# Kernel tuning notes

Hardware: AMD Instinct MI355X
Metric: run time of the kernel (lower is better)

The kernel has to match this reference:

```python
import jax, jax.numpy as jnp
import numpy as np

T, N, L = 2000, 128, 250
H, K, V, A = 512, 128, 128, 64  # hidden_dim, key_size, value_size, alphabet_size


def _lstm_cell(x, h, c, W_ih, W_hh, b_ih, b_hh):
    # PyTorch LSTMCell gate order: i, f, g, o
    gates = x @ W_ih.T + b_ih + h @ W_hh.T + b_hh
    i, f, g, o = jnp.split(gates, 4, axis=-1)
    c_new = jax.nn.sigmoid(f) * c + jax.nn.sigmoid(i) * jnp.tanh(g)
    h_new = jax.nn.sigmoid(o) * jnp.tanh(c_new)
    return h_new, c_new


def setup_inputs() -> dict:
    ks = jax.random.split(jax.random.key(0), 16)
    u = lambda k, shape, s: jax.random.uniform(k, shape, jnp.float32, -s, s)
    sH = 1.0 / np.sqrt(H)
    sK = 1.0 / np.sqrt(K)
    return {
        "key": jax.random.normal(ks[0], (T, N, K), jnp.float32),
        "values": jax.random.normal(ks[1], (T, N, V), jnp.float32),
        "lens": jax.random.randint(ks[2], (N,), 1, T + 1),
        "text": jax.random.randint(ks[3], (N, L), 0, A),
        "emb": jax.random.normal(ks[4], (A, H), jnp.float32).at[0].set(0.0),
        "W_ih1": u(ks[5], (4 * H, H + V), sH),
        "W_hh1": u(ks[6], (4 * H, H), sH),
        "b_ih1": u(ks[7], (4 * H,), sH),
        "b_hh1": u(ks[8], (4 * H,), sH),
        "W_ih2": u(ks[9], (4 * K, H), sK),
        "W_hh2": u(ks[10], (4 * K, K), sK),
        "b_ih2": u(ks[11], (4 * K,), sK),
        "b_hh2": u(ks[12], (4 * K,), sK),
        "W_mos": u(ks[13], (A, K + V), 1.0 / np.sqrt(K + V)),
        "b_mos": u(ks[14], (A,), 1.0 / np.sqrt(K + V)),
    }


def reference(key, values, lens, text, emb, W_ih1, W_hh1, b_ih1, b_hh1,
              W_ih2, W_hh2, b_ih2, b_hh2, W_mos, b_mos):
    batch = key.shape[1]
    # padding_idx=0: zero embedding for token 0
    embeddings = emb[text] * (text != 0)[..., None].astype(emb.dtype)  # (N,L,H)
    emb_seq = jnp.transpose(embeddings, (1, 0, 2))                     # (L,N,H)
    mask = jnp.arange(key.shape[0])[None, :] >= lens[:, None]          # (N,T)

    def step(carry, e):
        h1, c1, h2, c2, ctx = carry
        inp = jnp.concatenate([e, ctx], axis=1)                # (N,H+V)
        h1, c1 = _lstm_cell(inp, h1, c1, W_ih1, W_hh1, b_ih1, b_hh1)
        h2, c2 = _lstm_cell(h1, h2, c2, W_ih2, W_hh2, b_ih2, b_hh2)
        scores = jnp.einsum('tnk,nk->nt', key, h2)             # (N,T)
        scores = jnp.where(mask, -1e9, scores)
        attn = jax.nn.softmax(scores, axis=1)
        ctx = jnp.einsum('nt,tnv->nv', attn, values)           # (N,V)
        pred = jnp.concatenate([h2, ctx], axis=1) @ W_mos.T + b_mos  # (N,A)
        return (h1, c1, h2, c2, ctx), pred

    z1 = jnp.zeros((batch, H), key.dtype)
    z2 = jnp.zeros((batch, K), key.dtype)
    init = (z1, z1, z2, z2, values[0])
    _, preds = jax.lax.scan(step, init, emb_seq)               # (L,N,A)
    return jnp.transpose(preds, (1, 0, 2))                     # (N,L,A)
```

## Files before the change

### kernel.cpp

```cpp
#include <hip/hip_runtime.h>
#include <hip/hip_bf16.h>
#include <math.h>

#define T_ENC 2000
#define NB    128
#define LDEC  250
#define HDIM  512
#define KDIM  128
#define VDIM  128
#define ADIM  64
#define TC    100
#define NC    20
#define K1    1152
#define K2    640
#define N1    2048
#define N2    512

typedef __attribute__((ext_vector_type(8))) short bf16x8;
typedef __attribute__((ext_vector_type(4))) float f32x4;
typedef unsigned short u16;

__device__ __forceinline__ u16 f2bf(float x) {
    unsigned int b = __float_as_uint(x);
    b += 0x7fffu + ((b >> 16) & 1u);
    return (u16)(b >> 16);
}
__device__ __forceinline__ float bfhi2f(unsigned int u) {
    return __uint_as_float(u << 16);
}
__device__ __forceinline__ f32x4 mfma16(bf16x8 a, bf16x8 b, f32x4 c) {
    return __builtin_amdgcn_mfma_f32_16x16x32_bf16(a, b, c, 0, 0, 0);
}


__global__ void cvt_tr(const float* __restrict__ src, u16* __restrict__ dst) {
    size_t total = (size_t)T_ENC * NB * 128;
    for (size_t idx = (size_t)blockIdx.x * 256 + threadIdx.x; idx < total;
         idx += (size_t)gridDim.x * 256) {
        int t = idx >> 14;
        int n = (idx >> 7) & 127;
        int d = idx & 127;
        dst[((size_t)n * T_ENC + t) * 128 + d] = f2bf(src[idx]);
    }
}

__global__ void prep_emb(const int* __restrict__ text, const float* __restrict__ emb,
                         u16* __restrict__ Ehi, u16* __restrict__ Elo) {
    size_t total = (size_t)LDEC * NB * HDIM;
    for (size_t idx = (size_t)blockIdx.x * 256 + threadIdx.x; idx < total;
         idx += (size_t)gridDim.x * 256) {
        int t = idx >> 16;
        int n = (idx >> 9) & 127;
        int d = idx & 511;
        int tok = text[n * LDEC + t];
        float v = tok ? emb[(size_t)tok * HDIM + d] : 0.f;
        u16 hi = f2bf(v);
        Ehi[idx] = hi;
        Elo[idx] = f2bf(v - bfhi2f((unsigned int)hi));
    }
}

__global__ void prep_w1(const float* __restrict__ Wih, const float* __restrict__ Whh,
                        const float* __restrict__ bi, const float* __restrict__ bh,
                        u16* __restrict__ Whi, u16* __restrict__ Wlo,
                        float* __restrict__ bsum) {
    size_t total = (size_t)N1 * K1;
    for (size_t idx = (size_t)blockIdx.x * 256 + threadIdx.x; idx < total;
         idx += (size_t)gridDim.x * 256) {
        int c = idx / K1, k = idx % K1;
        float w = (k < 640) ? Wih[(size_t)c * 640 + k] : Whh[(size_t)c * 512 + (k - 640)];
        u16 hi = f2bf(w);
        Whi[idx] = hi;
        Wlo[idx] = f2bf(w - bfhi2f((unsigned int)hi));
    }
    int i = blockIdx.x * 256 + threadIdx.x;
    if (i < N1) bsum[i] = bi[i] + bh[i];
}

__global__ void prep_w2(const float* __restrict__ Wih, const float* __restrict__ Whh,
                        const float* __restrict__ bi, const float* __restrict__ bh,
                        u16* __restrict__ Whi, u16* __restrict__ Wlo,
                        float* __restrict__ bsum) {
    size_t total = (size_t)N2 * K2;
    for (size_t idx = (size_t)blockIdx.x * 256 + threadIdx.x; idx < total;
         idx += (size_t)gridDim.x * 256) {
        int c = idx / K2, k = idx % K2;
        float w = (k < 512) ? Wih[(size_t)c * 512 + k] : Whh[(size_t)c * 128 + (k - 512)];
        u16 hi = f2bf(w);
        Whi[idx] = hi;
        Wlo[idx] = f2bf(w - bfhi2f((unsigned int)hi));
    }
    int i = blockIdx.x * 256 + threadIdx.x;
    if (i < N2) bsum[i] = bi[i] + bh[i];
}

__global__ void init_state(float* c1, u16* h1hi, u16* h1lo,
                           float* c2, u16* h2hi, u16* h2lo,
                           u16* cxhi, u16* cxlo, const float* __restrict__ values) {
    int i = blockIdx.x * 256 + threadIdx.x;
    c1[i] = 0.f; h1hi[i] = 0; h1lo[i] = 0;
    if (i < NB * KDIM) {
        c2[i] = 0.f; h2hi[i] = 0; h2lo[i] = 0;
        float v = values[i];
        u16 hi = f2bf(v);
        cxhi[i] = hi; cxlo[i] = f2bf(v - bfhi2f((unsigned int)hi));
    }
}


__global__ __launch_bounds__(256) void lstm1_mfma(
    const u16* __restrict__ Ehi, const u16* __restrict__ Elo,
    const u16* __restrict__ cxhi, const u16* __restrict__ cxlo,
    const u16* __restrict__ h1hi, const u16* __restrict__ h1lo,
    const u16* __restrict__ W1hi, const u16* __restrict__ W1lo,
    float* __restrict__ gpart, int t)
{
    int tid = threadIdx.x, lane = tid & 63, wid = tid >> 6;
    int wn = wid >> 1, wj = wid & 1;
    int l15 = lane & 15, l4 = lane >> 4;
    int n0 = blockIdx.x * 64 + wn * 32;
    int j0 = blockIdx.y * 32 + wj * 16;
    int ks = blockIdx.z;
    int kbeg = ks * 288, kend = kbeg + 288;

    f32x4 zero = {0.f, 0.f, 0.f, 0.f};
    f32x4 acc[2][4];
#pragma unroll
    for (int m = 0; m < 2; ++m)
#pragma unroll
        for (int g = 0; g < 4; ++g) acc[m][g] = zero;

    size_t brow[4];
#pragma unroll
    for (int g = 0; g < 4; ++g) brow[g] = (size_t)(g * 512 + j0 + l15) * K1;
    int row0 = n0 + l15, row1 = n0 + 16 + l15;
    const u16* Et_hi = Ehi + (size_t)t * (NB * HDIM);
    const u16* Et_lo = Elo + (size_t)t * (NB * HDIM);

    for (int kk = kbeg; kk < kend; kk += 32) {
        int kb = kk + l4 * 8;
        const u16 *pah, *pal; size_t ao0, ao1;
        if (kk < 512) {
            pah = Et_hi; pal = Et_lo;
            ao0 = (size_t)row0 * 512 + kb; ao1 = (size_t)row1 * 512 + kb;
        } else if (kk < 640) {
            pah = cxhi; pal = cxlo;
            ao0 = (size_t)row0 * 128 + (kb - 512); ao1 = (size_t)row1 * 128 + (kb - 512);
        } else {
            pah = h1hi; pal = h1lo;
            ao0 = (size_t)row0 * 512 + (kb - 640); ao1 = (size_t)row1 * 512 + (kb - 640);
        }
        bf16x8 a0h = *(const bf16x8*)(pah + ao0);
        bf16x8 a0l = *(const bf16x8*)(pal + ao0);
        bf16x8 a1h = *(const bf16x8*)(pah + ao1);
        bf16x8 a1l = *(const bf16x8*)(pal + ao1);
#pragma unroll
        for (int g = 0; g < 4; ++g) {
            bf16x8 bh = *(const bf16x8*)(W1hi + brow[g] + kb);
            bf16x8 bl = *(const bf16x8*)(W1lo + brow[g] + kb);
            acc[0][g] = mfma16(a0h, bh, acc[0][g]);
            acc[0][g] = mfma16(a0h, bl, acc[0][g]);
            acc[0][g] = mfma16(a0l, bh, acc[0][g]);
            acc[1][g] = mfma16(a1h, bh, acc[1][g]);
            acc[1][g] = mfma16(a1h, bl, acc[1][g]);
            acc[1][g] = mfma16(a1l, bh, acc[1][g]);
        }
    }
#pragma unroll
    for (int mi = 0; mi < 2; ++mi)
#pragma unroll
        for (int g = 0; g < 4; ++g)
#pragma unroll
            for (int r = 0; r < 4; ++r) {
                int row = n0 + mi * 16 + l4 * 4 + r;
                gpart[((size_t)ks * NB + row) * N1 + g * 512 + j0 + l15] = acc[mi][g][r];
            }
}

__global__ __launch_bounds__(256) void pw1(
    const float* __restrict__ gpart, const float* __restrict__ bsum,
    float* __restrict__ c1, u16* __restrict__ h1hi, u16* __restrict__ h1lo)
{
    int idx = blockIdx.x * 256 + threadIdx.x;
    int n = idx >> 9, j = idx & 511;
    float g[4];
#pragma unroll
    for (int gi = 0; gi < 4; ++gi) {
        int c = gi * 512 + j;
        float s = bsum[c];
#pragma unroll
        for (int ks = 0; ks < 4; ++ks) s += gpart[((size_t)ks * NB + n) * N1 + c];
        g[gi] = s;
    }
    float cc = c1[idx];
    float i_ = 1.f / (1.f + expf(-g[0]));
    float f_ = 1.f / (1.f + expf(-g[1]));
    float g_ = tanhf(g[2]);
    float o_ = 1.f / (1.f + expf(-g[3]));
    float cn = f_ * cc + i_ * g_;
    c1[idx] = cn;
    float h = o_ * tanhf(cn);
    u16 hi = f2bf(h);
    h1hi[idx] = hi;
    h1lo[idx] = f2bf(h - bfhi2f((unsigned int)hi));
}

__global__ __launch_bounds__(256) void lstm2_mfma(
    const u16* __restrict__ h1hi, const u16* __restrict__ h1lo,
    const u16* __restrict__ h2hi, const u16* __restrict__ h2lo,
    const u16* __restrict__ W2hi, const u16* __restrict__ W2lo,
    float* __restrict__ gpart)
{
    int tid = threadIdx.x, lane = tid & 63, wid = tid >> 6;
    int wn = wid >> 1, wj = wid & 1;
    int l15 = lane & 15, l4 = lane >> 4;
    int n0 = blockIdx.x * 64 + wn * 32;
    int j0 = blockIdx.y * 32 + wj * 16;
    int ks = blockIdx.z;
    int kbeg = ks * 160, kend = kbeg + 160;

    f32x4 zero = {0.f, 0.f, 0.f, 0.f};
    f32x4 acc[2][4];
#pragma unroll
    for (int m = 0; m < 2; ++m)
#pragma unroll
        for (int g = 0; g < 4; ++g) acc[m][g] = zero;

    size_t brow[4];
#pragma unroll
    for (int g = 0; g < 4; ++g) brow[g] = (size_t)(g * 128 + j0 + l15) * K2;
    int row0 = n0 + l15, row1 = n0 + 16 + l15;

    for (int kk = kbeg; kk < kend; kk += 32) {
        int kb = kk + l4 * 8;
        const u16 *pah, *pal; size_t ao0, ao1;
        if (kk < 512) {
            pah = h1hi; pal = h1lo;
            ao0 = (size_t)row0 * 512 + kb; ao1 = (size_t)row1 * 512 + kb;
        } else {
            pah = h2hi; pal = h2lo;
            ao0 = (size_t)row0 * 128 + (kb - 512); ao1 = (size_t)row1 * 128 + (kb - 512);
        }
        bf16x8 a0h = *(const bf16x8*)(pah + ao0);
        bf16x8 a0l = *(const bf16x8*)(pal + ao0);
        bf16x8 a1h = *(const bf16x8*)(pah + ao1);
        bf16x8 a1l = *(const bf16x8*)(pal + ao1);
#pragma unroll
        for (int g = 0; g < 4; ++g) {
            bf16x8 bh = *(const bf16x8*)(W2hi + brow[g] + kb);
            bf16x8 bl = *(const bf16x8*)(W2lo + brow[g] + kb);
            acc[0][g] = mfma16(a0h, bh, acc[0][g]);
            acc[0][g] = mfma16(a0h, bl, acc[0][g]);
            acc[0][g] = mfma16(a0l, bh, acc[0][g]);
            acc[1][g] = mfma16(a1h, bh, acc[1][g]);
            acc[1][g] = mfma16(a1h, bl, acc[1][g]);
            acc[1][g] = mfma16(a1l, bh, acc[1][g]);
        }
    }
#pragma unroll
    for (int mi = 0; mi < 2; ++mi)
#pragma unroll
        for (int g = 0; g < 4; ++g)
#pragma unroll
            for (int r = 0; r < 4; ++r) {
                int row = n0 + mi * 16 + l4 * 4 + r;
                gpart[((size_t)ks * NB + row) * N2 + g * 128 + j0 + l15] = acc[mi][g][r];
            }
}

__global__ __launch_bounds__(256) void pw2(
    const float* __restrict__ gpart, const float* __restrict__ bsum,
    float* __restrict__ c2, float* __restrict__ h2f,
    u16* __restrict__ h2hi, u16* __restrict__ h2lo)
{
    int idx = blockIdx.x * 256 + threadIdx.x;
    int n = idx >> 7, j = idx & 127;
    float g[4];
#pragma unroll
    for (int gi = 0; gi < 4; ++gi) {
        int c = gi * 128 + j;
        float s = bsum[c];
#pragma unroll
        for (int ks = 0; ks < 4; ++ks) s += gpart[((size_t)ks * NB + n) * N2 + c];
        g[gi] = s;
    }
    float cc = c2[idx];
    float i_ = 1.f / (1.f + expf(-g[0]));
    float f_ = 1.f / (1.f + expf(-g[1]));
    float g_ = tanhf(g[2]);
    float o_ = 1.f / (1.f + expf(-g[3]));
    float cn = f_ * cc + i_ * g_;
    c2[idx] = cn;
    float h = o_ * tanhf(cn);
    h2f[idx] = h;
    u16 hi = f2bf(h);
    h2hi[idx] = hi;
    h2lo[idx] = f2bf(h - bfhi2f((unsigned int)hi));
}

__global__ __launch_bounds__(256) void attn_partial(
    const u16* __restrict__ kbf, const u16* __restrict__ vbf,
    const float* __restrict__ h2f, const int* __restrict__ lens,
    float* __restrict__ pmax, float* __restrict__ psum, float* __restrict__ pctx)
{
    int n = blockIdx.x, c = blockIdx.y, t0 = c * TC;
    int tid = threadIdx.x, lane = tid & 63, w = tid >> 6;
    int l15 = lane & 15, l4 = lane >> 4;
    __shared__ float pls[TC];
    __shared__ float red[8];
    __shared__ float cpart[4][VDIM];
    int len = lens[n];

    float h2r[8];
    {
        const float* hp = h2f + n * 128 + l15 * 8;
#pragma unroll
        for (int j = 0; j < 8; ++j) h2r[j] = hp[j];
    }

    const u16* kb_ = kbf + (size_t)n * T_ENC * 128;
    for (int q = w; q < 25; q += 4) {
        int tl = 4 * q + l4;
        int t = t0 + tl;
        uint4 u = *(const uint4*)(kb_ + (size_t)t * 128 + l15 * 8);
        float s = 0.f;
        s = fmaf(bfhi2f(u.x & 0xffffu), h2r[0], s);
        s = fmaf(bfhi2f(u.x >> 16),     h2r[1], s);
        s = fmaf(bfhi2f(u.y & 0xffffu), h2r[2], s);
        s = fmaf(bfhi2f(u.y >> 16),     h2r[3], s);
        s = fmaf(bfhi2f(u.z & 0xffffu), h2r[4], s);
        s = fmaf(bfhi2f(u.z >> 16),     h2r[5], s);
        s = fmaf(bfhi2f(u.w & 0xffffu), h2r[6], s);
        s = fmaf(bfhi2f(u.w >> 16),     h2r[7], s);
        s += __shfl_xor(s, 1, 64);
        s += __shfl_xor(s, 2, 64);
        s += __shfl_xor(s, 4, 64);
        s += __shfl_xor(s, 8, 64);
        if (t >= len) s = -1e30f;
        if (l15 == 0) pls[tl] = s;
    }
    __syncthreads();

    float m = -1e30f;
    for (int i = tid; i < TC; i += 256) m = fmaxf(m, pls[i]);
    for (int k = 32; k >= 1; k >>= 1) m = fmaxf(m, __shfl_xor(m, k, 64));
    if (lane == 0) red[w] = m;
    __syncthreads();
    m = fmaxf(fmaxf(red[0], red[1]), fmaxf(red[2], red[3]));
    bool empty = (m <= -1e29f);

    float ssum = 0.f;
    for (int i = tid; i < TC; i += 256) {
        float pv = empty ? 0.f : expf(pls[i] - m);
        pls[i] = pv;
        ssum += pv;
    }
    __syncthreads();
    for (int k = 32; k >= 1; k >>= 1) ssum += __shfl_xor(ssum, k, 64);
    if (lane == 0) red[4 + w] = ssum;
    __syncthreads();
    if (tid == 0) {
        pmax[n * NC + c] = empty ? -1e30f : m;
        psum[n * NC + c] = red[4] + red[5] + red[6] + red[7];
    }

    const u16* vb_ = vbf + (size_t)n * T_ENC * 128;
    int l5 = lane >> 5, l31 = lane & 31;
    float a4[4] = {0.f, 0.f, 0.f, 0.f};
    for (int p = w; p < 50; p += 4) {
        int tl = 2 * p + l5;
        int t = t0 + tl;
        float pv = pls[tl];
        uint2 u = *(const uint2*)(vb_ + (size_t)t * 128 + l31 * 4);
        a4[0] = fmaf(pv, bfhi2f(u.x & 0xffffu), a4[0]);
        a4[1] = fmaf(pv, bfhi2f(u.x >> 16),     a4[1]);
        a4[2] = fmaf(pv, bfhi2f(u.y & 0xffffu), a4[2]);
        a4[3] = fmaf(pv, bfhi2f(u.y >> 16),     a4[3]);
    }
#pragma unroll
    for (int j = 0; j < 4; ++j) a4[j] += __shfl_xor(a4[j], 32, 64);
    if (lane < 32) {
#pragma unroll
        for (int j = 0; j < 4; ++j) cpart[w][l31 * 4 + j] = a4[j];
    }
    __syncthreads();
    if (tid < 128)
        pctx[((size_t)n * NC + c) * VDIM + tid] =
            cpart[0][tid] + cpart[1][tid] + cpart[2][tid] + cpart[3][tid];
}

__global__ __launch_bounds__(64) void combine_pred(
    const float* __restrict__ pmax, const float* __restrict__ psum,
    const float* __restrict__ pctx, const float* __restrict__ h2f,
    u16* __restrict__ cxhi, u16* __restrict__ cxlo,
    const float* __restrict__ W_mos, const float* __restrict__ b_mos,
    float* __restrict__ out, int t)
{
    int n = blockIdx.x;
    int lane = threadIdx.x;

    float m = (lane < NC) ? pmax[n * NC + lane] : -1e30f;
    for (int k = 32; k >= 1; k >>= 1) m = fmaxf(m, __shfl_xor(m, k, 64));
    float s = (lane < NC) ? psum[n * NC + lane] * expf(pmax[n * NC + lane] - m) : 0.f;
    for (int k = 32; k >= 1; k >>= 1) s += __shfl_xor(s, k, 64);
    float inv = 1.f / s;

    __shared__ float xcat[2 * KDIM];
#pragma unroll
    for (int v2 = 0; v2 < 2; ++v2) {
        int v = lane + v2 * 64;
        float acc = 0.f;
        for (int c = 0; c < NC; ++c) {
            float e = expf(pmax[n * NC + c] - m);
            acc += pctx[((size_t)n * NC + c) * VDIM + v] * e;
        }
        acc *= inv;
        u16 hi = f2bf(acc);
        cxhi[n * 128 + v] = hi;
        cxlo[n * 128 + v] = f2bf(acc - bfhi2f((unsigned int)hi));
        xcat[KDIM + v] = acc;
    }
    xcat[lane] = h2f[n * 128 + lane];
    xcat[64 + lane] = h2f[n * 128 + 64 + lane];
    __syncthreads();

    float acc = b_mos[lane];
    const float* wr = W_mos + lane * (2 * KDIM);
#pragma unroll 4
    for (int i = 0; i < 2 * KDIM; ++i) acc += xcat[i] * wr[i];
    out[((size_t)n * LDEC + t) * ADIM + lane] = acc;
}


extern "C" void kernel_launch(void* const* d_in, const int* in_sizes, int n_in,
                              void* d_out, int out_size, void* d_ws, size_t ws_size,
                              hipStream_t stream)
{
    const float* key    = (const float*)d_in[0];
    const float* values = (const float*)d_in[1];
    const int*   lens   = (const int*)d_in[2];
    const int*   text   = (const int*)d_in[3];
    const float* emb    = (const float*)d_in[4];
    const float* W_ih1  = (const float*)d_in[5];
    const float* W_hh1  = (const float*)d_in[6];
    const float* b_ih1  = (const float*)d_in[7];
    const float* b_hh1  = (const float*)d_in[8];
    const float* W_ih2  = (const float*)d_in[9];
    const float* W_hh2  = (const float*)d_in[10];
    const float* b_ih2  = (const float*)d_in[11];
    const float* b_hh2  = (const float*)d_in[12];
    const float* W_mos  = (const float*)d_in[13];
    const float* b_mos  = (const float*)d_in[14];
    float* out = (float*)d_out;

    char* base = (char*)d_ws;
    size_t off = 0;
    auto alloc = [&](size_t bytes) -> char* {
        char* r = base + off;
        off += (bytes + 255) & ~(size_t)255;
        return r;
    };
    u16* kbf  = (u16*)alloc((size_t)T_ENC * NB * 128 * 2);
    u16* vbf  = (u16*)alloc((size_t)T_ENC * NB * 128 * 2);
    u16* Ehi  = (u16*)alloc((size_t)LDEC * NB * HDIM * 2);
    u16* Elo  = (u16*)alloc((size_t)LDEC * NB * HDIM * 2);
    u16* W1hi = (u16*)alloc((size_t)N1 * K1 * 2);
    u16* W1lo = (u16*)alloc((size_t)N1 * K1 * 2);
    u16* W2hi = (u16*)alloc((size_t)N2 * K2 * 2);
    u16* W2lo = (u16*)alloc((size_t)N2 * K2 * 2);
    float* bsum1 = (float*)alloc(N1 * 4);
    float* bsum2 = (float*)alloc(N2 * 4);
    float* gpart1 = (float*)alloc((size_t)4 * NB * N1 * 4);
    float* gpart2 = (float*)alloc((size_t)4 * NB * N2 * 4);
    u16* h1hiA = (u16*)alloc(NB * HDIM * 2);
    u16* h1loA = (u16*)alloc(NB * HDIM * 2);
    u16* h1hiB = (u16*)alloc(NB * HDIM * 2);
    u16* h1loB = (u16*)alloc(NB * HDIM * 2);
    u16* h2hiA = (u16*)alloc(NB * KDIM * 2);
    u16* h2loA = (u16*)alloc(NB * KDIM * 2);
    u16* h2hiB = (u16*)alloc(NB * KDIM * 2);
    u16* h2loB = (u16*)alloc(NB * KDIM * 2);
    float* c1  = (float*)alloc(NB * HDIM * 4);
    float* c2  = (float*)alloc(NB * KDIM * 4);
    float* h2f = (float*)alloc(NB * KDIM * 4);
    u16* cxhi = (u16*)alloc(NB * VDIM * 2);
    u16* cxlo = (u16*)alloc(NB * VDIM * 2);
    float* pmax = (float*)alloc(NB * NC * 4);
    float* psum = (float*)alloc(NB * NC * 4);
    float* pctx = (float*)alloc((size_t)NB * NC * VDIM * 4);
    (void)ws_size; (void)in_sizes; (void)n_in; (void)out_size;

    cvt_tr<<<4096, 256, 0, stream>>>(key, kbf);
    cvt_tr<<<4096, 256, 0, stream>>>(values, vbf);
    prep_emb<<<4096, 256, 0, stream>>>(text, emb, Ehi, Elo);
    prep_w1<<<2048, 256, 0, stream>>>(W_ih1, W_hh1, b_ih1, b_hh1, W1hi, W1lo, bsum1);
    prep_w2<<<512, 256, 0, stream>>>(W_ih2, W_hh2, b_ih2, b_hh2, W2hi, W2lo, bsum2);
    init_state<<<256, 256, 0, stream>>>(c1, h1hiA, h1loA, c2, h2hiA, h2loA,
                                        cxhi, cxlo, values);

    for (int t = 0; t < LDEC; ++t) {
        u16* h1hi_i = (t & 1) ? h1hiB : h1hiA;
        u16* h1lo_i = (t & 1) ? h1loB : h1loA;
        u16* h1hi_o = (t & 1) ? h1hiA : h1hiB;
        u16* h1lo_o = (t & 1) ? h1loA : h1loB;
        u16* h2hi_i = (t & 1) ? h2hiB : h2hiA;
        u16* h2lo_i = (t & 1) ? h2loB : h2loA;
        u16* h2hi_o = (t & 1) ? h2hiA : h2hiB;
        u16* h2lo_o = (t & 1) ? h2loA : h2loB;

        lstm1_mfma<<<dim3(2, 16, 4), 256, 0, stream>>>(
            Ehi, Elo, cxhi, cxlo, h1hi_i, h1lo_i, W1hi, W1lo, gpart1, t);
        pw1<<<256, 256, 0, stream>>>(gpart1, bsum1, c1, h1hi_o, h1lo_o);
        lstm2_mfma<<<dim3(2, 4, 4), 256, 0, stream>>>(
            h1hi_o, h1lo_o, h2hi_i, h2lo_i, W2hi, W2lo, gpart2);
        pw2<<<64, 256, 0, stream>>>(gpart2, bsum2, c2, h2f, h2hi_o, h2lo_o);
        attn_partial<<<dim3(NB, NC), 256, 0, stream>>>(kbf, vbf, h2f, lens,
                                                       pmax, psum, pctx);
        combine_pred<<<NB, 64, 0, stream>>>(pmax, psum, pctx, h2f,
                                            cxhi, cxlo, W_mos, b_mos, out, t);
    }
}
```

Before: 18.60 ms.

## Fuse LSTM gate GEMMs with pointwise cell update via in-block split-K reduction

Each LSTM layer's split-K GEMM now splits K across the four waves inside one block and reduces the partial sums in shared memory. The same block then applies the gate nonlinearities and updates the cell state. This removes the pw1 and pw2 launches and the global gpart round-trip on every decoder step, at the cost of a different grid shape and one block barrier. The attention partial kernel also exits early for chunks that lie entirely past the sequence length, which skips key loads and dot products for padded time steps.

```diff
diff --git a/kernel.cpp b/kernel.cpp
--- a/kernel.cpp
+++ b/kernel.cpp
@@ -108,20 +108,21 @@
 }
 
 
-__global__ __launch_bounds__(256) void lstm1_mfma(
+__global__ __launch_bounds__(256) void lstm1_fused(
     const u16* __restrict__ Ehi, const u16* __restrict__ Elo,
     const u16* __restrict__ cxhi, const u16* __restrict__ cxlo,
-    const u16* __restrict__ h1hi, const u16* __restrict__ h1lo,
+    const u16* __restrict__ h1hi_in, const u16* __restrict__ h1lo_in,
     const u16* __restrict__ W1hi, const u16* __restrict__ W1lo,
-    float* __restrict__ gpart, int t)
+    const float* __restrict__ bsum,
+    float* __restrict__ c1, u16* __restrict__ h1hi_o, u16* __restrict__ h1lo_o,
+    int t)
 {
-    int tid = threadIdx.x, lane = tid & 63, wid = tid >> 6;
-    int wn = wid >> 1, wj = wid & 1;
+    __shared__ float red[4][32][64];
+    int tid = threadIdx.x, lane = tid & 63, wk = tid >> 6;
     int l15 = lane & 15, l4 = lane >> 4;
-    int n0 = blockIdx.x * 64 + wn * 32;
-    int j0 = blockIdx.y * 32 + wj * 16;
-    int ks = blockIdx.z;
-    int kbeg = ks * 288, kend = kbeg + 288;
+    int n0 = blockIdx.x * 32;
+    int j0 = blockIdx.y * 16;
+    int kbeg = wk * 288, kend = kbeg + 288;
 
     f32x4 zero = {0.f, 0.f, 0.f, 0.f};
     f32x4 acc[2][4];
@@ -147,7 +148,7 @@
             pah = cxhi; pal = cxlo;
             ao0 = (size_t)row0 * 128 + (kb - 512); ao1 = (size_t)row1 * 128 + (kb - 512);
         } else {
-            pah = h1hi; pal = h1lo;
+            pah = h1hi_in; pal = h1lo_in;
             ao0 = (size_t)row0 * 512 + (kb - 640); ao1 = (size_t)row1 * 512 + (kb - 640);
         }
         bf16x8 a0h = *(const bf16x8*)(pah + ao0);
@@ -171,53 +172,49 @@
 #pragma unroll
         for (int g = 0; g < 4; ++g)
 #pragma unroll
-            for (int r = 0; r < 4; ++r) {
-                int row = n0 + mi * 16 + l4 * 4 + r;
-                gpart[((size_t)ks * NB + row) * N1 + g * 512 + j0 + l15] = acc[mi][g][r];
-            }
-}
-
-__global__ __launch_bounds__(256) void pw1(
-    const float* __restrict__ gpart, const float* __restrict__ bsum,
-    float* __restrict__ c1, u16* __restrict__ h1hi, u16* __restrict__ h1lo)
+            for (int r = 0; r < 4; ++r)
+                red[wk][mi * 16 + l4 * 4 + r][g * 16 + l15] = acc[mi][g][r];
+    __syncthreads();
+
+    for (int cell = tid; cell < 512; cell += 256) {
+        int nl = cell >> 4, jl = cell & 15;
+        float g[4];
+#pragma unroll
+        for (int gi = 0; gi < 4; ++gi) {
+            float s = bsum[gi * 512 + j0 + jl];
+#pragma unroll
+            for (int w = 0; w < 4; ++w) s += red[w][nl][gi * 16 + jl];
+            g[gi] = s;
+        }
+        int idx = (n0 + nl) * HDIM + j0 + jl;
+        float cc = c1[idx];
+        float i_ = 1.f / (1.f + expf(-g[0]));
+        float f_ = 1.f / (1.f + expf(-g[1]));
+        float g_ = tanhf(g[2]);
+        float o_ = 1.f / (1.f + expf(-g[3]));
+        float cn = f_ * cc + i_ * g_;
+        c1[idx] = cn;
+        float h = o_ * tanhf(cn);
+        u16 hi = f2bf(h);
+        h1hi_o[idx] = hi;
+        h1lo_o[idx] = f2bf(h - bfhi2f((unsigned int)hi));
+    }
+}
+
+__global__ __launch_bounds__(256) void lstm2_fused(
+    const u16* __restrict__ h1hi, const u16* __restrict__ h1lo,
+    const u16* __restrict__ h2hi_in, const u16* __restrict__ h2lo_in,
+    const u16* __restrict__ W2hi, const u16* __restrict__ W2lo,
+    const float* __restrict__ bsum,
+    float* __restrict__ c2, float* __restrict__ h2f,
+    u16* __restrict__ h2hi_o, u16* __restrict__ h2lo_o)
 {
-    int idx = blockIdx.x * 256 + threadIdx.x;
-    int n = idx >> 9, j = idx & 511;
-    float g[4];
-#pragma unroll
-    for (int gi = 0; gi < 4; ++gi) {
-        int c = gi * 512 + j;
-        float s = bsum[c];
-#pragma unroll
-        for (int ks = 0; ks < 4; ++ks) s += gpart[((size_t)ks * NB + n) * N1 + c];
-        g[gi] = s;
-    }
-    float cc = c1[idx];
-    float i_ = 1.f / (1.f + expf(-g[0]));
-    float f_ = 1.f / (1.f + expf(-g[1]));
-    float g_ = tanhf(g[2]);
-    float o_ = 1.f / (1.f + expf(-g[3]));
-    float cn = f_ * cc + i_ * g_;
-    c1[idx] = cn;
-    float h = o_ * tanhf(cn);
-    u16 hi = f2bf(h);
-    h1hi[idx] = hi;
-    h1lo[idx] = f2bf(h - bfhi2f((unsigned int)hi));
-}
-
-__global__ __launch_bounds__(256) void lstm2_mfma(
-    const u16* __restrict__ h1hi, const u16* __restrict__ h1lo,
-    const u16* __restrict__ h2hi, const u16* __restrict__ h2lo,
-    const u16* __restrict__ W2hi, const u16* __restrict__ W2lo,
-    float* __restrict__ gpart)
-{
-    int tid = threadIdx.x, lane = tid & 63, wid = tid >> 6;
-    int wn = wid >> 1, wj = wid & 1;
+    __shared__ float red[4][32][64];
+    int tid = threadIdx.x, lane = tid & 63, wk = tid >> 6;
     int l15 = lane & 15, l4 = lane >> 4;
-    int n0 = blockIdx.x * 64 + wn * 32;
-    int j0 = blockIdx.y * 32 + wj * 16;
-    int ks = blockIdx.z;
-    int kbeg = ks * 160, kend = kbeg + 160;
+    int n0 = blockIdx.x * 32;
+    int j0 = blockIdx.y * 16;
+    int kbeg = wk * 160, kend = kbeg + 160;
 
     f32x4 zero = {0.f, 0.f, 0.f, 0.f};
     f32x4 acc[2][4];
@@ -238,7 +235,7 @@
             pah = h1hi; pal = h1lo;
             ao0 = (size_t)row0 * 512 + kb; ao1 = (size_t)row1 * 512 + kb;
         } else {
-            pah = h2hi; pal = h2lo;
+            pah = h2hi_in; pal = h2lo_in;
             ao0 = (size_t)row0 * 128 + (kb - 512); ao1 = (size_t)row1 * 128 + (kb - 512);
         }
         bf16x8 a0h = *(const bf16x8*)(pah + ao0);
@@ -262,40 +259,34 @@
 #pragma unroll
         for (int g = 0; g < 4; ++g)
 #pragma unroll
-            for (int r = 0; r < 4; ++r) {
-                int row = n0 + mi * 16 + l4 * 4 + r;
-                gpart[((size_t)ks * NB + row) * N2 + g * 128 + j0 + l15] = acc[mi][g][r];
-            }
-}
-
-__global__ __launch_bounds__(256) void pw2(
-    const float* __restrict__ gpart, const float* __restrict__ bsum,
-    float* __restrict__ c2, float* __restrict__ h2f,
-    u16* __restrict__ h2hi, u16* __restrict__ h2lo)
-{
-    int idx = blockIdx.x * 256 + threadIdx.x;
-    int n = idx >> 7, j = idx & 127;
-    float g[4];
-#pragma unroll
-    for (int gi = 0; gi < 4; ++gi) {
-        int c = gi * 128 + j;
-        float s = bsum[c];
-#pragma unroll
-        for (int ks = 0; ks < 4; ++ks) s += gpart[((size_t)ks * NB + n) * N2 + c];
-        g[gi] = s;
-    }
-    float cc = c2[idx];
-    float i_ = 1.f / (1.f + expf(-g[0]));
-    float f_ = 1.f / (1.f + expf(-g[1]));
-    float g_ = tanhf(g[2]);
-    float o_ = 1.f / (1.f + expf(-g[3]));
-    float cn = f_ * cc + i_ * g_;
-    c2[idx] = cn;
-    float h = o_ * tanhf(cn);
-    h2f[idx] = h;
-    u16 hi = f2bf(h);
-    h2hi[idx] = hi;
-    h2lo[idx] = f2bf(h - bfhi2f((unsigned int)hi));
+            for (int r = 0; r < 4; ++r)
+                red[wk][mi * 16 + l4 * 4 + r][g * 16 + l15] = acc[mi][g][r];
+    __syncthreads();
+
+    for (int cell = tid; cell < 512; cell += 256) {
+        int nl = cell >> 4, jl = cell & 15;
+        float g[4];
+#pragma unroll
+        for (int gi = 0; gi < 4; ++gi) {
+            float s = bsum[gi * 128 + j0 + jl];
+#pragma unroll
+            for (int w = 0; w < 4; ++w) s += red[w][nl][gi * 16 + jl];
+            g[gi] = s;
+        }
+        int idx = (n0 + nl) * KDIM + j0 + jl;
+        float cc = c2[idx];
+        float i_ = 1.f / (1.f + expf(-g[0]));
+        float f_ = 1.f / (1.f + expf(-g[1]));
+        float g_ = tanhf(g[2]);
+        float o_ = 1.f / (1.f + expf(-g[3]));
+        float cn = f_ * cc + i_ * g_;
+        c2[idx] = cn;
+        float h = o_ * tanhf(cn);
+        h2f[idx] = h;
+        u16 hi = f2bf(h);
+        h2hi_o[idx] = hi;
+        h2lo_o[idx] = f2bf(h - bfhi2f((unsigned int)hi));
+    }
 }
 
 __global__ __launch_bounds__(256) void attn_partial(
@@ -306,10 +297,14 @@
     int n = blockIdx.x, c = blockIdx.y, t0 = c * TC;
     int tid = threadIdx.x, lane = tid & 63, w = tid >> 6;
     int l15 = lane & 15, l4 = lane >> 4;
+    int len = lens[n];
+    if (t0 >= len) {
+        if (tid == 0) { pmax[n * NC + c] = -1e30f; psum[n * NC + c] = 0.f; }
+        return;
+    }
     __shared__ float pls[TC];
     __shared__ float red[8];
     __shared__ float cpart[4][VDIM];
-    int len = lens[n];
 
     float h2r[8];
     {
@@ -347,11 +342,10 @@
     if (lane == 0) red[w] = m;
     __syncthreads();
     m = fmaxf(fmaxf(red[0], red[1]), fmaxf(red[2], red[3]));
-    bool empty = (m <= -1e29f);
 
     float ssum = 0.f;
     for (int i = tid; i < TC; i += 256) {
-        float pv = empty ? 0.f : expf(pls[i] - m);
+        float pv = expf(pls[i] - m);
         pls[i] = pv;
         ssum += pv;
     }
@@ -360,7 +354,7 @@
     if (lane == 0) red[4 + w] = ssum;
     __syncthreads();
     if (tid == 0) {
-        pmax[n * NC + c] = empty ? -1e30f : m;
+        pmax[n * NC + c] = m;
         psum[n * NC + c] = red[4] + red[5] + red[6] + red[7];
     }
 
@@ -470,8 +464,6 @@
     u16* W2lo = (u16*)alloc((size_t)N2 * K2 * 2);
     float* bsum1 = (float*)alloc(N1 * 4);
     float* bsum2 = (float*)alloc(N2 * 4);
-    float* gpart1 = (float*)alloc((size_t)4 * NB * N1 * 4);
-    float* gpart2 = (float*)alloc((size_t)4 * NB * N2 * 4);
     u16* h1hiA = (u16*)alloc(NB * HDIM * 2);
     u16* h1loA = (u16*)alloc(NB * HDIM * 2);
     u16* h1hiB = (u16*)alloc(NB * HDIM * 2);
@@ -508,12 +500,12 @@
         u16* h2hi_o = (t & 1) ? h2hiA : h2hiB;
         u16* h2lo_o = (t & 1) ? h2loA : h2loB;
 
-        lstm1_mfma<<<dim3(2, 16, 4), 256, 0, stream>>>(
-            Ehi, Elo, cxhi, cxlo, h1hi_i, h1lo_i, W1hi, W1lo, gpart1, t);
-        pw1<<<256, 256, 0, stream>>>(gpart1, bsum1, c1, h1hi_o, h1lo_o);
-        lstm2_mfma<<<dim3(2, 4, 4), 256, 0, stream>>>(
-            h1hi_o, h1lo_o, h2hi_i, h2lo_i, W2hi, W2lo, gpart2);
-        pw2<<<64, 256, 0, stream>>>(gpart2, bsum2, c2, h2f, h2hi_o, h2lo_o);
+        lstm1_fused<<<dim3(4, 32), 256, 0, stream>>>(
+            Ehi, Elo, cxhi, cxlo, h1hi_i, h1lo_i, W1hi, W1lo, bsum1,
+            c1, h1hi_o, h1lo_o, t);
+        lstm2_fused<<<dim3(4, 8), 256, 0, stream>>>(
+            h1hi_o, h1lo_o, h2hi_i, h2lo_i, W2hi, W2lo, bsum2,
+            c2, h2f, h2hi_o, h2lo_o);
         attn_partial<<<dim3(NB, NC), 256, 0, stream>>>(kbf, vbf, h2f, lens,
                                                        pmax, psum, pctx);
         combine_pred<<<NB, 64, 0, stream>>>(pmax, psum, pctx, h2f,
```

After: 15.76 ms. -15.2%, faster.
